# Kernel tuning notes

Hardware: AMD Instinct MI355X
Metric: run time of the kernel (lower is better)

## Reference

```python
import jax, jax.numpy as jnp
import numpy as np

B, N, F, H = 64, 1024, 128, 256  # graphs, nodes per graph, nfeat, nhid


def setup_inputs() -> dict:
    key = jax.random.key(0)
    ks = jax.random.split(key, 8)
    s_in = 1.0 / np.sqrt(F)
    s_h = 1.0 / np.sqrt(H)
    return {
        "embs": jax.random.normal(ks[0], (B, N, F), jnp.float32),
        "adjmat": jax.random.uniform(ks[1], (B, N, N), jnp.float32) / N,  # row-scaled dense adjacency
        "W0": jax.random.normal(ks[2], (F, H), jnp.float32) * s_in,
        "b0": jnp.zeros((H,), jnp.float32),
        "W1": jax.random.normal(ks[3], (H, H), jnp.float32) * s_h,
        "b1": jnp.zeros((H,), jnp.float32),
        "W2": jax.random.normal(ks[4], (H, H), jnp.float32) * s_h,
        "b2": jnp.zeros((H,), jnp.float32),
        "Wl": jax.random.normal(ks[5], (H, F), jnp.float32) * s_h,
        "bl": jnp.zeros((F,), jnp.float32),
    }


def reference(embs, adjmat, W0, b0, W1, b1, W2, b2, Wl, bl):
    # Batched form of the per-graph loop: every adj is N x N, so the
    # x[:adj.shape[0]] slice is identity and all graphs fuse into one GEMM.
    hid = embs  # [B, N, F]
    for W, b in ((W0, b0), (W1, b1), (W2, b2)):
        # GraphConvolution: adj @ (x @ W) + b, then relu
        hid = jax.nn.relu(jnp.einsum('bnm,bmh->bnh', adjmat, hid @ W) + b)
    out = hid @ Wl + bl          # [B, N, F] linear_hid
    return out[:, 0, :]          # hid[0] per graph -> [B, F]
```

## Files before the change

### kernel.cpp

```cpp
#include <hip/hip_runtime.h>
#include <stdint.h>

typedef __bf16 bf16;
typedef __bf16 bf16x8 __attribute__((ext_vector_type(8)));
typedef float f32x4 __attribute__((ext_vector_type(4)));

enum { EPI_STORE = 0, EPI_BIAS_RELU = 1, EPI_VRED = 2 };

__device__ __forceinline__ void load_lds16(const bf16* g, bf16* l) {
  __builtin_amdgcn_global_load_lds((const __attribute__((address_space(1))) void*)g,
                                   (__attribute__((address_space(3))) void*)l, 16, 0, 0);
}

template<int EPI>
__global__ __launch_bounds__(256, 3)
void gemm_bt(const bf16* __restrict__ Ap, const bf16* __restrict__ Btp,
             const float* __restrict__ bias, bf16* __restrict__ C,
             float* __restrict__ vpart, const bf16* __restrict__ a0p,
             int K, int ldA, int ldBt, int ldC,
             long sA, long sBt, long sC)
{
  constexpr int BM = 64, BN = 256, BK = 32;
  __shared__ __align__(16) bf16 As[BM * BK];
  __shared__ __align__(16) bf16 Bs[BN * BK];
  __shared__ float a0s[BM];
  __shared__ float vsum[BN];

  const int tid  = threadIdx.x;
  const int lane = tid & 63;
  const int wid  = tid >> 6;
  const int wm   = wid & 1;
  const int wn   = wid >> 1;
  const int l15  = lane & 15;
  const int quad = lane >> 4;

  const int nb = blockIdx.x, mb = blockIdx.y, g = blockIdx.z;

  const bf16* Ag = Ap + (long)g * sA + (long)(mb * BM + (tid >> 2)) * ldA + (tid & 3) * 8;
  const bf16* Bg = Btp + (long)g * sBt + (long)(nb * BN + (tid >> 2)) * ldBt + (tid & 3) * 8;
  const long bstep = (long)64 * ldBt;

  if constexpr (EPI == EPI_VRED) {
    if (tid < BM) a0s[tid] = (float)a0p[(long)g * sA + mb * BM + tid];
    vsum[tid] = 0.f;
  }

  f32x4 acc[2][8] = {};

  for (int ks = 0; ks < K; ks += BK) {
    __syncthreads();
    load_lds16(Ag + ks, As + tid * 8);
    #pragma unroll
    for (int p = 0; p < 4; ++p)
      load_lds16(Bg + p * bstep + ks, Bs + p * 2048 + tid * 8);
    __syncthreads();

    bf16x8 af[2], bfr[8];
    #pragma unroll
    for (int i = 0; i < 2; ++i)
      af[i] = *(const bf16x8*)&As[(wm * 32 + i * 16 + l15) * BK + quad * 8];
    #pragma unroll
    for (int j = 0; j < 8; ++j)
      bfr[j] = *(const bf16x8*)&Bs[(wn * 128 + j * 16 + l15) * BK + quad * 8];
    #pragma unroll
    for (int i = 0; i < 2; ++i)
      #pragma unroll
      for (int j = 0; j < 8; ++j)
        acc[i][j] = __builtin_amdgcn_mfma_f32_16x16x32_bf16(af[i], bfr[j], acc[i][j], 0, 0, 0);
  }

  if constexpr (EPI == EPI_STORE || EPI == EPI_BIAS_RELU) {
    bf16* Cg = C + (long)g * sC;
    #pragma unroll
    for (int i = 0; i < 2; ++i) {
      const int row0 = mb * BM + wm * 32 + i * 16 + quad * 4;
      #pragma unroll
      for (int j = 0; j < 8; ++j) {
        const int col = nb * BN + wn * 128 + j * 16 + l15;
        float bv = 0.f;
        if constexpr (EPI == EPI_BIAS_RELU) bv = bias[col];
        #pragma unroll
        for (int rr = 0; rr < 4; ++rr) {
          float v = acc[i][j][rr];
          if constexpr (EPI == EPI_BIAS_RELU) v = fmaxf(v + bv, 0.f);
          Cg[(long)(row0 + rr) * ldC + col] = (bf16)v;
        }
      }
    }
  } else {
    __syncthreads();
    #pragma unroll
    for (int j = 0; j < 8; ++j) {
      const int col = wn * 128 + j * 16 + l15;
      const float bv = bias[col];
      float p = 0.f;
      #pragma unroll
      for (int i = 0; i < 2; ++i) {
        const int lr = wm * 32 + i * 16 + quad * 4;
        #pragma unroll
        for (int rr = 0; rr < 4; ++rr)
          p += fmaxf(acc[i][j][rr] + bv, 0.f) * a0s[lr + rr];
      }
      atomicAdd(&vsum[col], p);
    }
    __syncthreads();
    vpart[((long)g * 16 + mb) * 256 + tid] = vsum[tid];
  }
}

__global__ void cvt_prep(const float* __restrict__ adj, const float* __restrict__ embs,
                         bf16* __restrict__ adjb, bf16* __restrict__ embsb)
{
  const long c = (long)blockIdx.x * 256 + threadIdx.x;
  const float* src; bf16* dst; long off;
  if (c < 8388608) { src = adj;  dst = adjb;  off = c * 8; }
  else             { src = embs; dst = embsb; off = (c - 8388608) * 8; }
  float4 v0 = *(const float4*)(src + off);
  float4 v1 = *(const float4*)(src + off + 4);
  bf16x8 w;
  w[0]=(bf16)v0.x; w[1]=(bf16)v0.y; w[2]=(bf16)v0.z; w[3]=(bf16)v0.w;
  w[4]=(bf16)v1.x; w[5]=(bf16)v1.y; w[6]=(bf16)v1.z; w[7]=(bf16)v1.w;
  *(bf16x8*)(dst + off) = w;
}

__global__ void prep_w(const float* __restrict__ W0, const float* __restrict__ W1,
                       bf16* __restrict__ W0t, bf16* __restrict__ W1t)
{
  const int idx = blockIdx.x * 256 + threadIdx.x;
  if (idx < 256 * 128) {
    const int h = idx >> 7, k = idx & 127;
    W0t[idx] = (bf16)W0[k * 256 + h];
  }
  const int h = idx >> 8, k = idx & 255;
  W1t[idx] = (bf16)W1[k * 256 + h];
}

__global__ void finish_k(const float* __restrict__ vpart, const float* __restrict__ W2,
                         const float* __restrict__ b2, const float* __restrict__ Wl,
                         const float* __restrict__ bl, float* __restrict__ out)
{
  const int b = blockIdx.x, t = threadIdx.x;
  __shared__ float v[256], h3[256];
  float s = 0.f;
  #pragma unroll
  for (int mb = 0; mb < 16; ++mb) s += vpart[((long)b * 16 + mb) * 256 + t];
  v[t] = s;
  __syncthreads();
  float z = b2[t];
  for (int k = 0; k < 256; ++k) z += v[k] * W2[k * 256 + t];
  h3[t] = fmaxf(z, 0.f);
  __syncthreads();
  if (t < 128) {
    float o = bl[t];
    for (int h = 0; h < 256; ++h) o += h3[h] * Wl[h * 128 + t];
    out[(long)b * 128 + t] = o;
  }
}

extern "C" void kernel_launch(void* const* d_in, const int* in_sizes, int n_in,
                              void* d_out, int out_size, void* d_ws, size_t ws_size,
                              hipStream_t stream) {
  const float* embs = (const float*)d_in[0];
  const float* adj  = (const float*)d_in[1];
  const float* W0   = (const float*)d_in[2];
  const float* b0   = (const float*)d_in[3];
  const float* W1   = (const float*)d_in[4];
  const float* b1   = (const float*)d_in[5];
  const float* W2   = (const float*)d_in[6];
  const float* b2   = (const float*)d_in[7];
  const float* Wl   = (const float*)d_in[8];
  const float* bl   = (const float*)d_in[9];
  float* out = (float*)d_out;

  char* ws = (char*)d_ws;
  bf16*  adjb  = (bf16*)(ws);
  bf16*  embsb = (bf16*)(ws + 134217728);
  bf16*  Zt    = (bf16*)(ws + 150994944);
  bf16*  Hb    = (bf16*)(ws + 184549376);
  bf16*  W0t   = (bf16*)(ws + 218103808);
  bf16*  W1t   = (bf16*)(ws + 218169344);
  float* vpart = (float*)(ws + 218300416);

  cvt_prep<<<36864, 256, 0, stream>>>(adj, embs, adjb, embsb);
  prep_w<<<256, 256, 0, stream>>>(W0, W1, W0t, W1t);

  gemm_bt<EPI_STORE><<<dim3(4, 4, 64), 256, 0, stream>>>(
      W0t, embsb, nullptr, Zt, nullptr, nullptr,
      128, 128, 128, 1024, 0L, 131072L, 262144L);

  gemm_bt<EPI_BIAS_RELU><<<dim3(1, 16, 64), 256, 0, stream>>>(
      adjb, Zt, b0, Hb, nullptr, nullptr,
      1024, 1024, 1024, 256, 1048576L, 262144L, 262144L);

  gemm_bt<EPI_STORE><<<dim3(4, 4, 64), 256, 0, stream>>>(
      W1t, Hb, nullptr, Zt, nullptr, nullptr,
      256, 256, 256, 1024, 0L, 262144L, 262144L);

  gemm_bt<EPI_VRED><<<dim3(1, 16, 64), 256, 0, stream>>>(
      adjb, Zt, b1, nullptr, vpart, adjb,
      1024, 1024, 1024, 256, 1048576L, 262144L, 0L);

  finish_k<<<64, 256, 0, stream>>>(vpart, W2, b2, Wl, bl, out);
}
```

Before: 619.7 us.

## Restructure GEMM to 128x128 tiles with per-wave double-buffered async LDS loads

Replaces the 64x256 block tile with a 128x128 tile where each wave owns a private 64x64 sub-tile and stages its own A/B slices into LDS. Loads are double-buffered with explicit vmcnt/lgkmcnt waits instead of block-wide __syncthreads per K step, so global loads for step s+2 overlap MFMA work. Grid shapes, launch bounds, and the VRED partial reduction layout (8 row blocks, 2 column blocks) change to match. Per-wave private tiles cut cross-wave data sharing, which raises global/L2 traffic per FLOP. The prefetch also wraps modulo nsteps and issues redundant loads at the tail.

```diff
diff --git a/kernel.cpp b/kernel.cpp
--- a/kernel.cpp
+++ b/kernel.cpp
@@ -13,70 +13,76 @@
 }
 
 template<int EPI>
-__global__ __launch_bounds__(256, 3)
+__global__ __launch_bounds__(256, 2)
 void gemm_bt(const bf16* __restrict__ Ap, const bf16* __restrict__ Btp,
              const float* __restrict__ bias, bf16* __restrict__ C,
              float* __restrict__ vpart, const bf16* __restrict__ a0p,
              int K, int ldA, int ldBt, int ldC,
              long sA, long sBt, long sC)
 {
-  constexpr int BM = 64, BN = 256, BK = 32;
-  __shared__ __align__(16) bf16 As[BM * BK];
-  __shared__ __align__(16) bf16 Bs[BN * BK];
-  __shared__ float a0s[BM];
-  __shared__ float vsum[BN];
+  __shared__ __align__(16) bf16 As[4][2][64 * 32];
+  __shared__ __align__(16) bf16 Bs[4][2][64 * 32];
 
   const int tid  = threadIdx.x;
   const int lane = tid & 63;
   const int wid  = tid >> 6;
-  const int wm   = wid & 1;
-  const int wn   = wid >> 1;
+  const int wm   = wid >> 1;
+  const int wn   = wid & 1;
   const int l15  = lane & 15;
   const int quad = lane >> 4;
 
   const int nb = blockIdx.x, mb = blockIdx.y, g = blockIdx.z;
 
-  const bf16* Ag = Ap + (long)g * sA + (long)(mb * BM + (tid >> 2)) * ldA + (tid & 3) * 8;
-  const bf16* Bg = Btp + (long)g * sBt + (long)(nb * BN + (tid >> 2)) * ldBt + (tid & 3) * 8;
-  const long bstep = (long)64 * ldBt;
-
-  if constexpr (EPI == EPI_VRED) {
-    if (tid < BM) a0s[tid] = (float)a0p[(long)g * sA + mb * BM + tid];
-    vsum[tid] = 0.f;
-  }
-
-  f32x4 acc[2][8] = {};
-
-  for (int ks = 0; ks < K; ks += BK) {
-    __syncthreads();
-    load_lds16(Ag + ks, As + tid * 8);
-    #pragma unroll
-    for (int p = 0; p < 4; ++p)
-      load_lds16(Bg + p * bstep + ks, Bs + p * 2048 + tid * 8);
-    __syncthreads();
-
-    bf16x8 af[2], bfr[8];
-    #pragma unroll
-    for (int i = 0; i < 2; ++i)
-      af[i] = *(const bf16x8*)&As[(wm * 32 + i * 16 + l15) * BK + quad * 8];
-    #pragma unroll
-    for (int j = 0; j < 8; ++j)
-      bfr[j] = *(const bf16x8*)&Bs[(wn * 128 + j * 16 + l15) * BK + quad * 8];
-    #pragma unroll
-    for (int i = 0; i < 2; ++i)
-      #pragma unroll
-      for (int j = 0; j < 8; ++j)
+  const int lr = lane >> 2;
+  const int lk = (lane & 3) * 8;
+
+  const bf16* Ag = Ap  + (long)g * sA  + (long)(mb * 128 + wm * 64 + lr) * ldA  + lk;
+  const bf16* Bg = Btp + (long)g * sBt + (long)(nb * 128 + wn * 64 + lr) * ldBt + lk;
+
+  auto stage = [&](int st, int kt) {
+    const int k0 = kt * 32;
+    #pragma unroll
+    for (int t = 0; t < 4; ++t)
+      load_lds16(Ag + (long)t * 16 * ldA + k0, &As[wid][st][t * 512 + lane * 8]);
+    #pragma unroll
+    for (int t = 0; t < 4; ++t)
+      load_lds16(Bg + (long)t * 16 * ldBt + k0, &Bs[wid][st][t * 512 + lane * 8]);
+  };
+
+  f32x4 acc[4][4] = {};
+  const int nsteps = K / 32;
+
+  stage(0, 0);
+  stage(1, 1 % nsteps);
+
+  for (int s = 0; s < nsteps; ++s) {
+    asm volatile("s_waitcnt vmcnt(8)" ::: "memory");
+    const int st = s & 1;
+    bf16x8 af[4], bfr[4];
+    #pragma unroll
+    for (int i = 0; i < 4; ++i)
+      af[i] = *(const bf16x8*)&As[wid][st][(i * 16 + l15) * 32 + quad * 8];
+    #pragma unroll
+    for (int j = 0; j < 4; ++j)
+      bfr[j] = *(const bf16x8*)&Bs[wid][st][(j * 16 + l15) * 32 + quad * 8];
+    asm volatile("s_waitcnt lgkmcnt(0)" ::: "memory");
+    stage(st, (s + 2) % nsteps);
+    #pragma unroll
+    for (int i = 0; i < 4; ++i)
+      #pragma unroll
+      for (int j = 0; j < 4; ++j)
         acc[i][j] = __builtin_amdgcn_mfma_f32_16x16x32_bf16(af[i], bfr[j], acc[i][j], 0, 0, 0);
   }
+  asm volatile("s_waitcnt vmcnt(0)" ::: "memory");
 
   if constexpr (EPI == EPI_STORE || EPI == EPI_BIAS_RELU) {
     bf16* Cg = C + (long)g * sC;
     #pragma unroll
-    for (int i = 0; i < 2; ++i) {
-      const int row0 = mb * BM + wm * 32 + i * 16 + quad * 4;
-      #pragma unroll
-      for (int j = 0; j < 8; ++j) {
-        const int col = nb * BN + wn * 128 + j * 16 + l15;
+    for (int i = 0; i < 4; ++i) {
+      const int row0 = mb * 128 + wm * 64 + i * 16 + quad * 4;
+      #pragma unroll
+      for (int j = 0; j < 4; ++j) {
+        const int col = nb * 128 + wn * 64 + j * 16 + l15;
         float bv = 0.f;
         if constexpr (EPI == EPI_BIAS_RELU) bv = bias[col];
         #pragma unroll
@@ -88,23 +94,32 @@
       }
     }
   } else {
+    const bf16* a0g = a0p + (long)g * sA + mb * 128 + wm * 64;
+    float a0v[4][4];
+    #pragma unroll
+    for (int i = 0; i < 4; ++i)
+      #pragma unroll
+      for (int rr = 0; rr < 4; ++rr)
+        a0v[i][rr] = (float)a0g[i * 16 + quad * 4 + rr];
     __syncthreads();
-    #pragma unroll
-    for (int j = 0; j < 8; ++j) {
-      const int col = wn * 128 + j * 16 + l15;
-      const float bv = bias[col];
+    float* vsum = (float*)&As[0][0][0];
+    if (tid < 128) vsum[tid] = 0.f;
+    __syncthreads();
+    #pragma unroll
+    for (int j = 0; j < 4; ++j) {
+      const int lcol = wn * 64 + j * 16 + l15;
+      const float bv = bias[nb * 128 + lcol];
       float p = 0.f;
       #pragma unroll
-      for (int i = 0; i < 2; ++i) {
-        const int lr = wm * 32 + i * 16 + quad * 4;
+      for (int i = 0; i < 4; ++i)
         #pragma unroll
         for (int rr = 0; rr < 4; ++rr)
-          p += fmaxf(acc[i][j][rr] + bv, 0.f) * a0s[lr + rr];
-      }
-      atomicAdd(&vsum[col], p);
+          p += fmaxf(acc[i][j][rr] + bv, 0.f) * a0v[i][rr];
+      atomicAdd(&vsum[lcol], p);
     }
     __syncthreads();
-    vpart[((long)g * 16 + mb) * 256 + tid] = vsum[tid];
+    if (tid < 128)
+      vpart[((long)g * 8 + mb) * 256 + nb * 128 + tid] = vsum[tid];
   }
 }
 
@@ -143,7 +158,7 @@
   __shared__ float v[256], h3[256];
   float s = 0.f;
   #pragma unroll
-  for (int mb = 0; mb < 16; ++mb) s += vpart[((long)b * 16 + mb) * 256 + t];
+  for (int mb = 0; mb < 8; ++mb) s += vpart[((long)b * 8 + mb) * 256 + t];
   v[t] = s;
   __syncthreads();
   float z = b2[t];
@@ -184,19 +199,19 @@
   cvt_prep<<<36864, 256, 0, stream>>>(adj, embs, adjb, embsb);
   prep_w<<<256, 256, 0, stream>>>(W0, W1, W0t, W1t);
 
-  gemm_bt<EPI_STORE><<<dim3(4, 4, 64), 256, 0, stream>>>(
+  gemm_bt<EPI_STORE><<<dim3(8, 2, 64), 256, 0, stream>>>(
       W0t, embsb, nullptr, Zt, nullptr, nullptr,
       128, 128, 128, 1024, 0L, 131072L, 262144L);
 
-  gemm_bt<EPI_BIAS_RELU><<<dim3(1, 16, 64), 256, 0, stream>>>(
+  gemm_bt<EPI_BIAS_RELU><<<dim3(2, 8, 64), 256, 0, stream>>>(
       adjb, Zt, b0, Hb, nullptr, nullptr,
       1024, 1024, 1024, 256, 1048576L, 262144L, 262144L);
 
-  gemm_bt<EPI_STORE><<<dim3(4, 4, 64), 256, 0, stream>>>(
+  gemm_bt<EPI_STORE><<<dim3(8, 2, 64), 256, 0, stream>>>(
       W1t, Hb, nullptr, Zt, nullptr, nullptr,
       256, 256, 256, 1024, 0L, 262144L, 262144L);
 
-  gemm_bt<EPI_VRED><<<dim3(1, 16, 64), 256, 0, stream>>>(
+  gemm_bt<EPI_VRED><<<dim3(2, 8, 64), 256, 0, stream>>>(
       adjb, Zt, b1, nullptr, vpart, adjb,
       1024, 1024, 1024, 256, 1048576L, 262144L, 0L);
 
```

Result: no change. 627.3 us (+1.2%).
